# Optimization experiments

Hardware: AMD Instinct MI355X
Metric: run time of the kernel (lower is better)

Reference implementation:

```python
import jax, jax.numpy as jnp
from jax import lax
import numpy as np

T, B, IN, H = 192, 16, 256, 256


def setup_inputs() -> dict:
    key = jax.random.key(0)
    ks = jax.random.split(key, 8)
    s = 0.05  # small init scale to keep gates well-conditioned
    return {
        "x": jax.random.normal(ks[0], (T, B, IN), dtype=jnp.float32),
        # shared LSTM (PyTorch gate order i,f,g,o)
        "W_ih": jax.random.normal(ks[1], (4 * H, IN), dtype=jnp.float32) * s,
        "W_hh": jax.random.normal(ks[2], (4 * H, H), dtype=jnp.float32) * s,
        "b_lstm": jnp.zeros((4 * H,), dtype=jnp.float32),
        # additive attention: Ws: (IN+2H)->H, Us: H->1
        "Ws_w": jax.random.normal(ks[3], (H, IN + 2 * H), dtype=jnp.float32) * s,
        "Ws_b": jnp.zeros((H,), dtype=jnp.float32),
        "Us_w": jax.random.normal(ks[4], (1, H), dtype=jnp.float32) * s,
        "Us_b": jnp.zeros((1,), dtype=jnp.float32),
        # task-specific message LSTM cell: gates from concat(x_t, Rt, h_prev)
        "Wc": jax.random.normal(ks[5], (4 * H, IN + 2 * H), dtype=jnp.float32) * s,
        "bc": jnp.zeros((4 * H,), dtype=jnp.float32),
        "TASK": 0,
    }


def _lstm_gates(pre, c):
    i, f, g, o = jnp.split(pre, 4, axis=-1)
    i = jax.nn.sigmoid(i)
    f = jax.nn.sigmoid(f)
    g = jnp.tanh(g)
    o = jax.nn.sigmoid(o)
    c_new = f * c + i * g
    h_new = o * jnp.tanh(c_new)
    return h_new, c_new


def reference(x, W_ih, W_hh, b_lstm, Ws_w, Ws_b, Us_w, Us_b, Wc, bc, TASK):
    t_len, b, _ = x.shape
    h = W_hh.shape[1]

    h0 = jnp.zeros((b, h), x.dtype)

    # ---- shared LSTM over time ----
    def shared_step(carry, xt):
        hh, cc = carry
        pre = xt @ W_ih.T + hh @ W_hh.T + b_lstm
        hh, cc = _lstm_gates(pre, cc)
        return (hh, cc), hh

    (_, _), hs = lax.scan(shared_step, (h0, h0), x)  # hs: [T,B,H]

    # ---- per-timestep additive attention + message LSTM cell ----
    def task_step(carry, xt):
        hh, cc = carry
        h_task = jnp.broadcast_to(hh[None], (t_len, b, h))
        cat = jnp.concatenate([hs, h_task, x], axis=-1)          # [T,B,IN+2H]
        score = jnp.tanh(cat @ Ws_w.T + Ws_b) @ Us_w.T + Us_b    # [T,B,1]
        att = jax.nn.softmax(score, axis=0)                       # over time
        Rt = jnp.sum(att * hs, axis=0)                            # [B,H]
        pre = jnp.concatenate([xt, Rt, hh], axis=-1) @ Wc.T + bc
        hh, cc = _lstm_gates(pre, cc)
        return (hh, cc), hh

    (_, _), outs = lax.scan(task_step, (h0, h0), x)  # [T,B,H]
    return jnp.transpose(outs, (1, 0, 2))  # [B,T,H] (torch.stack axis=1)
```

## Files before the change

kernel.cpp:

```cpp
#include <hip/hip_runtime.h>
#include <hip/hip_fp16.h>

#define T_LEN 192

typedef unsigned long long u64;
typedef _Float16 f16x8 __attribute__((ext_vector_type(8)));
typedef float f32x4 __attribute__((ext_vector_type(4)));

#define OFF_X1F   0
#define OFF_XPRE  3145728
#define OFF_XB3   6291456
#define OFF_HSB   7077888
#define OFF_P     7864320
#define OFF_H     7921664
#define OFF_HX    7929856
#define OFF_HP    7946240
#define EXCH_WORDS 147456

#define SMEM_TASK 148736

__device__ __forceinline__ unsigned packh2(float a, float b){
  union { __half2 h; unsigned u; } v;
  v.h = __halves2half2(__float2half(a), __float2half(b));
  return v.u;
}
__device__ __forceinline__ float2 unp2(unsigned u){
  union { unsigned u32; __half2 h; } v; v.u32 = u;
  return __half22float2(v.h);
}
__device__ __forceinline__ float fdot2(unsigned a, unsigned b, float c){
#if __has_builtin(__builtin_amdgcn_fdot2)
  typedef _Float16 h2t __attribute__((ext_vector_type(2)));
  union { unsigned u; h2t h; } ua, ub;
  ua.u = a; ub.u = b;
  return __builtin_amdgcn_fdot2(ua.h, ub.h, c, false);
#else
  float2 x = unp2(a), y = unp2(b);
  return c + x.x*y.x + x.y*y.y;
#endif
}
__device__ __forceinline__ float tanh_f(float x){
  float cx = fminf(fmaxf(x, -15.f), 15.f);
  float e = __expf(2.f * cx);
  return (e - 1.f) / (e + 1.f);
}
__device__ __forceinline__ float sigm(float x){
  float cx = fminf(fmaxf(x, -30.f), 30.f);
  return 1.f / (1.f + __expf(-cx));
}

__device__ __forceinline__ u64 gld64(const u64* p){
  return __hip_atomic_load(p, __ATOMIC_RELAXED, __HIP_MEMORY_SCOPE_AGENT);
}
__device__ __forceinline__ void gst64(u64* p, u64 v){
  __hip_atomic_store(p, v, __ATOMIC_RELAXED, __HIP_MEMORY_SCOPE_AGENT);
}

__global__ __launch_bounds__(256) void initk(float* p, int n){
  int i = blockIdx.x * blockDim.x + threadIdx.x;
  int stride = gridDim.x * blockDim.x;
  for (; i < n; i += stride) p[i] = 0.f;
}

__global__ __launch_bounds__(256) void proj3m(const float* __restrict__ x,
                                              const float* __restrict__ W_ih,
                                              const float* __restrict__ b_l,
                                              const float* __restrict__ Wc,
                                              const float* __restrict__ bc,
                                              const float* __restrict__ Ws_w,
                                              const float* __restrict__ Ws_b,
                                              float* __restrict__ ws){
  __shared__ unsigned xhi[2][16 * 136];
  __shared__ unsigned xlo[2][16 * 136];
  const int bx = blockIdx.x, t0 = blockIdx.y * 2, tid = threadIdx.x;

  #pragma unroll
  for (int tt = 0; tt < 2; ++tt) {
    int row = tid >> 4, c0 = (tid & 15) * 16;
    const float* xp = &x[((t0 + tt) * 16 + row) * 256 + c0];
    #pragma unroll
    for (int i = 0; i < 8; ++i) {
      float2 v = *(const float2*)&xp[2 * i];
      _Float16 h0 = (_Float16)v.x, h1 = (_Float16)v.y;
      float l0 = v.x - (float)h0, l1 = v.y - (float)h1;
      union { _Float16 h[2]; unsigned u; } ph, pl;
      ph.h[0] = h0; ph.h[1] = h1;
      pl.h[0] = (_Float16)l0; pl.h[1] = (_Float16)l1;
      xhi[tt][row * 136 + c0 / 2 + i] = ph.u;
      xlo[tt][row * 136 + c0 / 2 + i] = pl.u;
    }
  }

  const int wave = tid >> 6, lane = tid & 63;
  const int b16 = lane & 15, quad = lane >> 4;
  const int n0 = bx * 64 + wave * 16;
  const float* wrow; const float* bias; int nb, mode;
  if (bx < 16)      { nb = n0;        wrow = &W_ih[(nb + b16) * 256];       bias = b_l;  mode = 0; }
  else if (bx < 32) { nb = n0 - 1024; wrow = &Wc[(nb + b16) * 768];         bias = bc;   mode = 1; }
  else              { nb = n0 - 2048; wrow = &Ws_w[(nb + b16) * 768 + 512]; bias = Ws_b; mode = 2; }

  f16x8 whi[8], wlo[8];
  #pragma unroll
  for (int kk = 0; kk < 8; ++kk) {
    const float* wp = wrow + kk * 32 + quad * 8;
    f16x8 h, l;
    #pragma unroll
    for (int j = 0; j < 8; ++j) {
      float v = wp[j];
      _Float16 hh = (_Float16)v;
      h[j] = hh; l[j] = (_Float16)(v - (float)hh);
    }
    whi[kk] = h; wlo[kk] = l;
  }
  f32x4 acc[2];
  #pragma unroll
  for (int tt = 0; tt < 2; ++tt)
    #pragma unroll
    for (int r = 0; r < 4; ++r) acc[tt][r] = bias[nb + quad * 4 + r];
  __syncthreads();

  #pragma unroll
  for (int kk = 0; kk < 8; ++kk) {
    #pragma unroll
    for (int tt = 0; tt < 2; ++tt) {
      union { uint4 u; f16x8 h; } bh, bl;
      bh.u = *(const uint4*)&xhi[tt][b16 * 136 + kk * 16 + quad * 4];
      bl.u = *(const uint4*)&xlo[tt][b16 * 136 + kk * 16 + quad * 4];
      acc[tt] = __builtin_amdgcn_mfma_f32_16x16x32_f16(whi[kk], bh.h, acc[tt], 0, 0, 0);
      acc[tt] = __builtin_amdgcn_mfma_f32_16x16x32_f16(wlo[kk], bh.h, acc[tt], 0, 0, 0);
      acc[tt] = __builtin_amdgcn_mfma_f32_16x16x32_f16(whi[kk], bl.h, acc[tt], 0, 0, 0);
    }
  }

  #pragma unroll
  for (int tt = 0; tt < 2; ++tt) {
    int t = t0 + tt;
    float4 res; res.x = acc[tt][0]; res.y = acc[tt][1]; res.z = acc[tt][2]; res.w = acc[tt][3];
    if (mode == 0) {
      *(float4*)&ws[OFF_X1F + (((u64)t * 64 + (n0 >> 4)) * 16 + b16) * 16 + quad * 4] = res;
    } else if (mode == 1) {
      *(float4*)&ws[OFF_XPRE + ((u64)t * 16 + b16) * 1024 + nb + quad * 4] = res;
    } else {
      *(float4*)&ws[OFF_XB3 + ((u64)t * 16 + b16) * 256 + nb + quad * 4] = res;
    }
  }
}

__global__ __launch_bounds__(512) void lstm_kernel(const float* __restrict__ X1F,
                                                   const float* __restrict__ W_hh,
                                                   float* __restrict__ hsB,
                                                   u64* __restrict__ hx){
  __shared__ unsigned hT[16 * 136];
  const int tid = threadIdx.x;
  const int wg = blockIdx.x;
  const int wave = tid >> 6, lane = tid & 63;
  const int b16 = lane & 15, quad = lane >> 4;
  const int jb = wg * 8 + wave;
  const int peerbase = (1 - wg) * 64;

  f16x8 wf[4][8];
  #pragma unroll
  for (int g = 0; g < 4; ++g) {
    #pragma unroll
    for (int kk = 0; kk < 8; ++kk) {
      int row = g * 256 + jb * 16 + b16;
      const float* wp = &W_hh[row * 256 + kk * 32 + quad * 8];
      f16x8 v;
      #pragma unroll
      for (int j = 0; j < 8; ++j) v[j] = (_Float16)wp[j];
      wf[g][kk] = v;
    }
  }
  for (int i = tid; i < 16 * 136; i += 512) hT[i] = 0u;
  float cst[4] = {0.f, 0.f, 0.f, 0.f};
  __syncthreads();

  for (int t = 0; t < T_LEN; ++t) {
    float4 xi[4];
    #pragma unroll
    for (int g = 0; g < 4; ++g)
      xi[g] = *(const float4*)&X1F[((t * 64 + g * 16 + jb) * 16 + b16) * 16 + quad * 4];

    if (t > 0) {
      const u64* src = &hx[((u64)((t - 1) & 1)) * 2048];
      int bbq = tid >> 5, k2 = tid & 31;
      int jp0 = peerbase + 2 * k2;
      u64 v0 = gld64(&src[bbq * 128 + jp0]);
      u64 v1 = gld64(&src[bbq * 128 + jp0 + 1]);
      while ((unsigned)v0 != (unsigned)t || (unsigned)v1 != (unsigned)t) {
        __builtin_amdgcn_s_sleep(1);
        v0 = gld64(&src[bbq * 128 + jp0]);
        v1 = gld64(&src[bbq * 128 + jp0 + 1]);
      }
      hT[bbq * 136 + jp0]     = (unsigned)(v0 >> 32);
      hT[bbq * 136 + jp0 + 1] = (unsigned)(v1 >> 32);
    }
    __syncthreads();

    f32x4 acc[4];
    #pragma unroll
    for (int g = 0; g < 4; ++g) {
      f32x4 a; a[0]=xi[g].x; a[1]=xi[g].y; a[2]=xi[g].z; a[3]=xi[g].w;
      acc[g] = a;
    }
    #pragma unroll
    for (int kk = 0; kk < 8; ++kk) {
      union { uint4 u; f16x8 h; } bv;
      bv.u = *(const uint4*)&hT[b16 * 136 + kk * 16 + quad * 4];
      #pragma unroll
      for (int g = 0; g < 4; ++g)
        acc[g] = __builtin_amdgcn_mfma_f32_16x16x32_f16(wf[g][kk], bv.h, acc[g], 0, 0, 0);
    }
    __syncthreads();

    float hv[4];
    #pragma unroll
    for (int r = 0; r < 4; ++r) {
      float pi = acc[0][r], pf = acc[1][r], pg = acc[2][r], po = acc[3][r];
      float cn = fmaf(sigm(pf), cst[r], sigm(pi) * tanh_f(pg));
      hv[r] = sigm(po) * tanh_f(cn);
      cst[r] = cn;
    }
    int j0 = jb * 16 + quad * 4;
    int jp = j0 >> 1;
    unsigned p01 = packh2(hv[0], hv[1]);
    unsigned p23 = packh2(hv[2], hv[3]);
    u64* dst = &hx[((u64)(t & 1)) * 2048];
    gst64(&dst[b16 * 128 + jp],     ((u64)p01 << 32) | (unsigned)(t + 1));
    gst64(&dst[b16 * 128 + jp + 1], ((u64)p23 << 32) | (unsigned)(t + 1));
    *(float4*)&hsB[(b16 * 192 + t) * 256 + j0] = make_float4(hv[0], hv[1], hv[2], hv[3]);
    hT[b16 * 136 + jp]     = p01;
    hT[b16 * 136 + jp + 1] = p23;
  }
}

__global__ __launch_bounds__(1024) void task_kernel(
    const float* __restrict__ xb3, const float* __restrict__ xpre,
    const float* __restrict__ hsB, const float* __restrict__ Us_w,
    const float* __restrict__ Us_b, const float* __restrict__ Wc,
    const float* __restrict__ Ws_w,
    u64* __restrict__ Pbuf, u64* __restrict__ Hbuf, u64* __restrict__ HPbuf,
    float* __restrict__ out){
  extern __shared__ char smem[];
  unsigned* hsL  = (unsigned*)smem;
  unsigned* Ws1L = (unsigned*)(smem + 99072);
  float*    baseS= (float*)(smem + 115584);
  unsigned* WcH  = (unsigned*)smem;
  unsigned* Ws2P = (unsigned*)(smem + 65536);
  float* prel    = (float*)(smem + 82944);
  float* eel     = (float*)(smem + 89600);
  unsigned* h2l  = (unsigned*)(smem + 90368);
  unsigned* h2own= (unsigned*)(smem + 90880);
  float* hterml  = (float*)(smem + 90944);
  float* usl     = (float*)(smem + 91072);
  float* msc     = (float*)(smem + 91200);
  unsigned* G2   = (unsigned*)(smem + 99072);

  const int tid = threadIdx.x;
  const int bb = blockIdx.x & 15;
  const int s  = blockIdx.x >> 4;

  for (int idx = tid; idx < 24576; idx += 1024) {
    int tp = idx >> 7, k2 = idx & 127;
    const float* hp = &hsB[(bb * 192 + tp) * 256 + 2 * k2];
    hsL[tp * 129 + k2] = packh2(hp[0], hp[1]);
  }
  for (int idx = tid; idx < 4096; idx += 1024) {
    int c = idx >> 7, k2 = idx & 127;
    const float* wp = &Ws_w[(32 * s + c) * 768 + 2 * k2];
    Ws1L[c * 129 + k2] = packh2(wp[0], wp[1]);
  }
  __syncthreads();
  {
    int c = tid & 31, g = tid >> 5;
    float a6[6];
    #pragma unroll
    for (int j = 0; j < 6; ++j)
      a6[j] = xb3[((g * 6 + j) * 16 + bb) * 256 + 32 * s + c];
    for (int k2 = 0; k2 < 128; ++k2) {
      unsigned wv = Ws1L[c * 129 + k2];
      #pragma unroll
      for (int j = 0; j < 6; ++j)
        a6[j] = fdot2(wv, hsL[(g * 6 + j) * 129 + k2], a6[j]);
    }
    #pragma unroll
    for (int j = 0; j < 6; ++j)
      baseS[(g * 6 + j) * 33 + c] = a6[j];
  }
  __syncthreads();
  unsigned bs4[4] = {0u, 0u, 0u, 0u};
  if (tid < 768) {
    int tp = tid >> 2, q = tid & 3;
    #pragma unroll
    for (int j2 = 0; j2 < 4; ++j2)
      bs4[j2] = packh2(baseS[tp * 33 + q * 8 + 2 * j2],
                       baseS[tp * 33 + q * 8 + 2 * j2 + 1]);
  }
  __syncthreads();
  {
    int l = tid & 127, tg = tid >> 7;
    int row = (l >> 5) * 256 + 32 * s + (l & 31);
    const float* wr = &Wc[row * 768 + 256];
    float acc[24];
    #pragma unroll
    for (int i = 0; i < 24; ++i) acc[i] = 0.f;
    for (int kc = 0; kc < 128; kc += 16) {
      unsigned wv[16];
      #pragma unroll
      for (int i = 0; i < 16; ++i) {
        float2 wp2 = *(const float2*)&wr[2 * (kc + i)];
        wv[i] = packh2(wp2.x, wp2.y);
      }
      #pragma unroll
      for (int tt = 0; tt < 24; ++tt) {
        const unsigned* hp = &hsL[(tg * 24 + tt) * 129 + kc];
        float a = acc[tt];
        #pragma unroll
        for (int i = 0; i < 16; ++i) a = fdot2(wv[i], hp[i], a);
        acc[tt] = a;
      }
    }
    #pragma unroll
    for (int i = 0; i < 12; ++i)
      G2[l * 97 + tg * 12 + i] = packh2(acc[2 * i], acc[2 * i + 1]);
  }
  __syncthreads();
  for (int idx = tid; idx < 16384; idx += 1024) {
    int j = idx & 3, l = (idx >> 2) & 127, k2q = idx >> 9;
    int k2 = k2q * 4 + j;
    int row = (l >> 5) * 256 + 32 * s + (l & 31);
    const float* wp = &Wc[row * 768 + 512 + 2 * k2];
    WcH[idx] = packh2(wp[0], wp[1]);
  }
  for (int idx = tid; idx < 4096; idx += 1024) {
    int c = idx >> 4, j = idx & 15;
    const float* wp = &Ws_w[c * 768 + 256 + 2 * (16 * s + j)];
    Ws2P[c * 17 + j] = packh2(wp[0], wp[1]);
  }
  if (tid < 32) usl[tid] = Us_w[32 * s + tid];
  const float usb = Us_b[0];
  __syncthreads();

  u64* Pb  = Pbuf + (bb * 8) * 192;
  u64* Hb  = Hbuf + bb * 256;
  u64* HPb = HPbuf + (bb * 8) * 256;
  const uint4* wp4 = (const uint4*)WcH;
  const uint4* av4 = (const uint4*)h2l;
  float creg = 0.f;

  for (int t = 0; t < T_LEN; ++t) {
    const unsigned seq = (unsigned)(t + 1);
    float xp0 = 0.f, xp1 = 0.f, xp2 = 0.f, xp3 = 0.f;
    if (tid < 32) {
      const float* xq = &xpre[(t * 16 + bb) * 1024 + 32 * s + tid];
      xp0 = xq[0]; xp1 = xq[256]; xp2 = xq[512]; xp3 = xq[768];
    }
    if (t > 0) {
      if (tid < 256) {
        int c = tid >> 3, sp = tid & 7;
        u64 v = gld64(&HPb[sp * 256 + 32 * s + c]);
        while ((unsigned)v != (unsigned)t) {
          __builtin_amdgcn_s_sleep(1);
          v = gld64(&HPb[sp * 256 + 32 * s + c]);
        }
        float a = __uint_as_float((unsigned)(v >> 32));
        a += __shfl_xor(a, 1); a += __shfl_xor(a, 2); a += __shfl_xor(a, 4);
        if (sp == 0) hterml[c] = a;
      } else if (tid < 512) {
        int col = tid - 256;
        u64 v = gld64(&Hb[col]);
        while ((unsigned)v != (unsigned)t) {
          __builtin_amdgcn_s_sleep(1);
          v = gld64(&Hb[col]);
        }
        float hvv = __uint_as_float((unsigned)(v >> 32));
        float hp_ = __shfl_xor(hvv, 1);
        if ((col & 1) == 0) h2l[col >> 1] = packh2(hvv, hp_);
      }
    } else {
      if (tid < 32) hterml[tid] = 0.f;
      if (tid < 128) h2l[tid] = 0u;
    }
    __syncthreads();
    if (tid < 768) {
      int tp = tid >> 2, q = tid & 3;
      float p = 0.f;
      #pragma unroll
      for (int m = 0; m < 4; ++m) {
        float2 bv = unp2(bs4[m]);
        int c0 = q * 8 + 2 * m;
        p += usl[c0]     * tanh_f(bv.x + hterml[c0]);
        p += usl[c0 + 1] * tanh_f(bv.y + hterml[c0 + 1]);
      }
      p += __shfl_xor(p, 1);
      p += __shfl_xor(p, 2);
      if ((tid & 3) == 0)
        gst64(&Pb[s * 192 + tp], ((u64)__float_as_uint(p) << 32) | seq);
    }
    {
      int l = tid & 127, kq = tid >> 7;
      float a = 0.f;
      #pragma unroll
      for (int i = 0; i < 4; ++i) {
        uint4 w4 = wp4[(kq * 4 + i) * 128 + l];
        uint4 a4 = av4[kq * 4 + i];
        a = fdot2(w4.x, a4.x, a); a = fdot2(w4.y, a4.y, a);
        a = fdot2(w4.z, a4.z, a); a = fdot2(w4.w, a4.w, a);
      }
      prel[l * 13 + kq] = a;
    }
    if (tid < 192) {
      u64 v[8];
      for (;;) {
        bool ok = true;
        #pragma unroll
        for (int sp = 0; sp < 8; ++sp) {
          v[sp] = gld64(&Pb[sp * 192 + tid]);
          ok &= ((unsigned)v[sp] == seq);
        }
        if (ok) break;
        __builtin_amdgcn_s_sleep(1);
      }
      float sum = 0.f;
      #pragma unroll
      for (int sp = 0; sp < 8; ++sp) sum += __uint_as_float((unsigned)(v[sp] >> 32));
      eel[tid] = __expf(sum + usb);
    }
    __syncthreads();
    if (tid < 64) {
      float aa = eel[tid] + eel[tid + 64] + eel[tid + 128];
      #pragma unroll
      for (int off = 32; off >= 1; off >>= 1) aa += __shfl_xor(aa, off);
      if (tid == 0) msc[0] = 1.f / aa;
    }
    if (tid >= 512) {
      int l = (tid - 512) & 127, tq = (tid - 512) >> 7;
      const unsigned* gp = &G2[l * 97 + tq * 24];
      const float2* ep = (const float2*)&eel[tq * 48];
      float a = 0.f;
      #pragma unroll
      for (int i = 0; i < 24; ++i) {
        float2 g = unp2(gp[i]);
        float2 e = ep[i];
        a = fmaf(g.x, e.x, a); a = fmaf(g.y, e.y, a);
      }
      prel[l * 13 + 8 + tq] = a;
    }
    __syncthreads();
    if (tid < 32) {
      float m = msc[0];
      float pr[4];
      #pragma unroll
      for (int g = 0; g < 4; ++g) {
        const float* pp = &prel[(g * 32 + tid) * 13];
        float hsum = pp[0] + pp[1] + pp[2] + pp[3] + pp[4] + pp[5] + pp[6] + pp[7];
        float gsum = pp[8] + pp[9] + pp[10] + pp[11];
        pr[g] = hsum + m * gsum;
      }
      pr[0] += xp0; pr[1] += xp1; pr[2] += xp2; pr[3] += xp3;
      float cn = fmaf(sigm(pr[1]), creg, sigm(pr[0]) * tanh_f(pr[2]));
      float hh = sigm(pr[3]) * tanh_f(cn);
      creg = cn;
      gst64(&Hb[32 * s + tid], ((u64)__float_as_uint(hh) << 32) | seq);
      out[(bb * 192 + t) * 256 + 32 * s + tid] = hh;
      float hp_ = __shfl_xor(hh, 1);
      if ((tid & 1) == 0) h2own[tid >> 1] = packh2(hh, hp_);
    }
    __syncthreads();
    if (tid < 256) {
      float a = 0.f;
      const unsigned* wp = &Ws2P[tid * 17];
      #pragma unroll
      for (int j = 0; j < 16; ++j) a = fdot2(wp[j], h2own[j], a);
      gst64(&HPb[s * 256 + tid], ((u64)__float_as_uint(a) << 32) | seq);
    }
  }
}

extern "C" void kernel_launch(void* const* d_in, const int* in_sizes, int n_in,
                              void* d_out, int out_size, void* d_ws, size_t ws_size,
                              hipStream_t stream) {
  (void)in_sizes; (void)n_in; (void)out_size; (void)ws_size;
  const float* x    = (const float*)d_in[0];
  const float* W_ih = (const float*)d_in[1];
  const float* W_hh = (const float*)d_in[2];
  const float* b_l  = (const float*)d_in[3];
  const float* Ws_w = (const float*)d_in[4];
  const float* Ws_b = (const float*)d_in[5];
  const float* Us_w = (const float*)d_in[6];
  const float* Us_b = (const float*)d_in[7];
  const float* Wc   = (const float*)d_in[8];
  const float* bc   = (const float*)d_in[9];
  float* out = (float*)d_out;
  float* ws = (float*)d_ws;

  hipFuncSetAttribute((const void*)task_kernel,
                      hipFuncAttributeMaxDynamicSharedMemorySize, 160 * 1024);

  initk<<<64, 256, 0, stream>>>(ws + OFF_P, EXCH_WORDS);

  proj3m<<<dim3(36, 96), 256, 0, stream>>>(x, W_ih, b_l, Wc, bc, Ws_w, Ws_b, ws);

  lstm_kernel<<<2, 512, 0, stream>>>(ws + OFF_X1F, W_hh, ws + OFF_HSB,
                                     (u64*)(ws + OFF_HX));

  task_kernel<<<128, 1024, SMEM_TASK, stream>>>(
      ws + OFF_XB3, ws + OFF_XPRE, ws + OFF_HSB, Us_w, Us_b, Wc, Ws_w,
      (u64*)(ws + OFF_P), (u64*)(ws + OFF_H), (u64*)(ws + OFF_HP), out);
}
```

Before: 1.630 ms.

## Co-locate LSTM workgroups on one XCD and poll flags with sc0 loads

```diff
diff --git a/kernel.cpp b/kernel.cpp
--- a/kernel.cpp
+++ b/kernel.cpp
@@ -14,6 +14,7 @@
 #define OFF_P     7864320
 #define OFF_H     7921664
 #define OFF_HX    7929856
+#define OFF_TICKET 7938048
 #define OFF_HP    7946240
 #define EXCH_WORDS 147456
 
@@ -54,6 +55,30 @@
 }
 __device__ __forceinline__ void gst64(u64* p, u64 v){
   __hip_atomic_store(p, v, __ATOMIC_RELAXED, __HIP_MEMORY_SCOPE_AGENT);
+}
+__device__ __forceinline__ u64 ld64_sc0(const u64* p){
+  u64 v;
+  asm volatile("global_load_dwordx2 %0, %1, off sc0\n\ts_waitcnt vmcnt(0)"
+               : "=v"(v) : "v"(p) : "memory");
+  return v;
+}
+__device__ __forceinline__ void st64_sc0(u64* p, u64 v){
+  asm volatile("global_store_dwordx2 %0, %1, off sc0" :: "v"(p), "v"(v) : "memory");
+}
+__device__ __forceinline__ void pub64(u64* p, u64 v){
+  gst64(p, v);
+  st64_sc0(p, v);
+}
+__device__ __forceinline__ u64 poll_tag(const u64* p, unsigned want){
+  for (int k = 1; ; ++k) {
+    u64 v = ld64_sc0(p);
+    if ((unsigned)v == want) return v;
+    if ((k & 7) == 0) {
+      v = gld64(p);
+      if ((unsigned)v == want) return v;
+      __builtin_amdgcn_s_sleep(1);
+    }
+  }
 }
 
 __global__ __launch_bounds__(256) void initk(float* p, int n){
@@ -149,10 +174,35 @@
 __global__ __launch_bounds__(512) void lstm_kernel(const float* __restrict__ X1F,
                                                    const float* __restrict__ W_hh,
                                                    float* __restrict__ hsB,
-                                                   u64* __restrict__ hx){
+                                                   u64* __restrict__ hx,
+                                                   unsigned* __restrict__ ticket){
   __shared__ unsigned hT[16 * 136];
+  __shared__ int role_s;
   const int tid = threadIdx.x;
-  const int wg = blockIdx.x;
+
+  if (tid == 0) {
+    int xcc = (int)__builtin_amdgcn_s_getreg(20 | (31 << 11)) & 7;
+    unsigned slot = __hip_atomic_fetch_add(&ticket[xcc], 1u,
+                        __ATOMIC_RELAXED, __HIP_MEMORY_SCOPE_AGENT);
+    int role = -1;
+    if (slot < 2u) {
+      if (slot == 1u) {
+        unsigned expv = 0u;
+        __hip_atomic_compare_exchange_strong(&ticket[8], &expv, (unsigned)(xcc + 1),
+            __ATOMIC_RELAXED, __ATOMIC_RELAXED, __HIP_MEMORY_SCOPE_AGENT);
+      }
+      unsigned ch;
+      do {
+        ch = __hip_atomic_load(&ticket[8], __ATOMIC_RELAXED, __HIP_MEMORY_SCOPE_AGENT);
+      } while (ch == 0u);
+      if (ch == (unsigned)(xcc + 1)) role = (int)slot;
+    }
+    role_s = role;
+  }
+  __syncthreads();
+  const int wg = role_s;
+  if (wg < 0) return;
+
   const int wave = tid >> 6, lane = tid & 63;
   const int b16 = lane & 15, quad = lane >> 4;
   const int jb = wg * 8 + wave;
@@ -185,12 +235,17 @@
       const u64* src = &hx[((u64)((t - 1) & 1)) * 2048];
       int bbq = tid >> 5, k2 = tid & 31;
       int jp0 = peerbase + 2 * k2;
-      u64 v0 = gld64(&src[bbq * 128 + jp0]);
-      u64 v1 = gld64(&src[bbq * 128 + jp0 + 1]);
-      while ((unsigned)v0 != (unsigned)t || (unsigned)v1 != (unsigned)t) {
-        __builtin_amdgcn_s_sleep(1);
-        v0 = gld64(&src[bbq * 128 + jp0]);
-        v1 = gld64(&src[bbq * 128 + jp0 + 1]);
+      const u64* ap = &src[bbq * 128 + jp0];
+      u64 v0, v1;
+      for (int k = 1; ; ++k) {
+        v0 = ld64_sc0(ap);
+        v1 = ld64_sc0(ap + 1);
+        if ((unsigned)v0 == (unsigned)t && (unsigned)v1 == (unsigned)t) break;
+        if ((k & 7) == 0) {
+          v0 = gld64(ap); v1 = gld64(ap + 1);
+          if ((unsigned)v0 == (unsigned)t && (unsigned)v1 == (unsigned)t) break;
+          __builtin_amdgcn_s_sleep(1);
+        }
       }
       hT[bbq * 136 + jp0]     = (unsigned)(v0 >> 32);
       hT[bbq * 136 + jp0 + 1] = (unsigned)(v1 >> 32);
@@ -226,8 +281,13 @@
     unsigned p01 = packh2(hv[0], hv[1]);
     unsigned p23 = packh2(hv[2], hv[3]);
     u64* dst = &hx[((u64)(t & 1)) * 2048];
-    gst64(&dst[b16 * 128 + jp],     ((u64)p01 << 32) | (unsigned)(t + 1));
-    gst64(&dst[b16 * 128 + jp + 1], ((u64)p23 << 32) | (unsigned)(t + 1));
+    u64* ap = &dst[b16 * 128 + jp];
+    u64 r0 = ((u64)p01 << 32) | (unsigned)(t + 1);
+    u64 r1 = ((u64)p23 << 32) | (unsigned)(t + 1);
+    gst64(ap, r0);
+    gst64(ap + 1, r1);
+    st64_sc0(ap, r0);
+    st64_sc0(ap + 1, r1);
     *(float4*)&hsB[(b16 * 192 + t) * 256 + j0] = make_float4(hv[0], hv[1], hv[2], hv[3]);
     hT[b16 * 136 + jp]     = p01;
     hT[b16 * 136 + jp + 1] = p23;
@@ -358,21 +418,13 @@
     if (t > 0) {
       if (tid < 256) {
         int c = tid >> 3, sp = tid & 7;
-        u64 v = gld64(&HPb[sp * 256 + 32 * s + c]);
-        while ((unsigned)v != (unsigned)t) {
-          __builtin_amdgcn_s_sleep(1);
-          v = gld64(&HPb[sp * 256 + 32 * s + c]);
-        }
+        u64 v = poll_tag(&HPb[sp * 256 + 32 * s + c], (unsigned)t);
         float a = __uint_as_float((unsigned)(v >> 32));
         a += __shfl_xor(a, 1); a += __shfl_xor(a, 2); a += __shfl_xor(a, 4);
         if (sp == 0) hterml[c] = a;
       } else if (tid < 512) {
         int col = tid - 256;
-        u64 v = gld64(&Hb[col]);
-        while ((unsigned)v != (unsigned)t) {
-          __builtin_amdgcn_s_sleep(1);
-          v = gld64(&Hb[col]);
-        }
+        u64 v = poll_tag(&Hb[col], (unsigned)t);
         float hvv = __uint_as_float((unsigned)(v >> 32));
         float hp_ = __shfl_xor(hvv, 1);
         if ((col & 1) == 0) h2l[col >> 1] = packh2(hvv, hp_);
@@ -395,7 +447,7 @@
       p += __shfl_xor(p, 1);
       p += __shfl_xor(p, 2);
       if ((tid & 3) == 0)
-        gst64(&Pb[s * 192 + tp], ((u64)__float_as_uint(p) << 32) | seq);
+        pub64(&Pb[s * 192 + tp], ((u64)__float_as_uint(p) << 32) | seq);
     }
     {
       int l = tid & 127, kq = tid >> 7;
@@ -410,20 +462,51 @@
       prel[l * 13 + kq] = a;
     }
     if (tid < 192) {
-      u64 v[8];
-      for (;;) {
-        bool ok = true;
-        #pragma unroll
-        for (int sp = 0; sp < 8; ++sp) {
-          v[sp] = gld64(&Pb[sp * 192 + tid]);
-          ok &= ((unsigned)v[sp] == seq);
+      const u64 *q0 = &Pb[0 * 192 + tid], *q1 = &Pb[1 * 192 + tid];
+      const u64 *q2 = &Pb[2 * 192 + tid], *q3 = &Pb[3 * 192 + tid];
+      const u64 *q4 = &Pb[4 * 192 + tid], *q5 = &Pb[5 * 192 + tid];
+      const u64 *q6 = &Pb[6 * 192 + tid], *q7 = &Pb[7 * 192 + tid];
+      u64 v0, v1, v2, v3, v4, v5, v6, v7;
+      for (int k = 1; ; ++k) {
+        asm volatile(
+          "global_load_dwordx2 %0, %8, off sc0\n\t"
+          "global_load_dwordx2 %1, %9, off sc0\n\t"
+          "global_load_dwordx2 %2, %10, off sc0\n\t"
+          "global_load_dwordx2 %3, %11, off sc0\n\t"
+          "global_load_dwordx2 %4, %12, off sc0\n\t"
+          "global_load_dwordx2 %5, %13, off sc0\n\t"
+          "global_load_dwordx2 %6, %14, off sc0\n\t"
+          "global_load_dwordx2 %7, %15, off sc0\n\t"
+          "s_waitcnt vmcnt(0)"
+          : "=&v"(v0), "=&v"(v1), "=&v"(v2), "=&v"(v3),
+            "=&v"(v4), "=&v"(v5), "=&v"(v6), "=&v"(v7)
+          : "v"(q0), "v"(q1), "v"(q2), "v"(q3),
+            "v"(q4), "v"(q5), "v"(q6), "v"(q7)
+          : "memory");
+        bool ok = (unsigned)v0 == seq && (unsigned)v1 == seq &&
+                  (unsigned)v2 == seq && (unsigned)v3 == seq &&
+                  (unsigned)v4 == seq && (unsigned)v5 == seq &&
+                  (unsigned)v6 == seq && (unsigned)v7 == seq;
+        if (ok) break;
+        if ((k & 7) == 0) {
+          v0 = gld64(q0); v1 = gld64(q1); v2 = gld64(q2); v3 = gld64(q3);
+          v4 = gld64(q4); v5 = gld64(q5); v6 = gld64(q6); v7 = gld64(q7);
+          ok = (unsigned)v0 == seq && (unsigned)v1 == seq &&
+               (unsigned)v2 == seq && (unsigned)v3 == seq &&
+               (unsigned)v4 == seq && (unsigned)v5 == seq &&
+               (unsigned)v6 == seq && (unsigned)v7 == seq;
+          if (ok) break;
+          __builtin_amdgcn_s_sleep(1);
         }
-        if (ok) break;
-        __builtin_amdgcn_s_sleep(1);
-      }
-      float sum = 0.f;
-      #pragma unroll
-      for (int sp = 0; sp < 8; ++sp) sum += __uint_as_float((unsigned)(v[sp] >> 32));
+      }
+      float sum = __uint_as_float((unsigned)(v0 >> 32)) +
+                  __uint_as_float((unsigned)(v1 >> 32)) +
+                  __uint_as_float((unsigned)(v2 >> 32)) +
+                  __uint_as_float((unsigned)(v3 >> 32)) +
+                  __uint_as_float((unsigned)(v4 >> 32)) +
+                  __uint_as_float((unsigned)(v5 >> 32)) +
+                  __uint_as_float((unsigned)(v6 >> 32)) +
+                  __uint_as_float((unsigned)(v7 >> 32));
       eel[tid] = __expf(sum + usb);
     }
     __syncthreads();
@@ -461,7 +544,7 @@
       float cn = fmaf(sigm(pr[1]), creg, sigm(pr[0]) * tanh_f(pr[2]));
       float hh = sigm(pr[3]) * tanh_f(cn);
       creg = cn;
-      gst64(&Hb[32 * s + tid], ((u64)__float_as_uint(hh) << 32) | seq);
+      pub64(&Hb[32 * s + tid], ((u64)__float_as_uint(hh) << 32) | seq);
       out[(bb * 192 + t) * 256 + 32 * s + tid] = hh;
       float hp_ = __shfl_xor(hh, 1);
       if ((tid & 1) == 0) h2own[tid >> 1] = packh2(hh, hp_);
@@ -472,7 +555,7 @@
       const unsigned* wp = &Ws2P[tid * 17];
       #pragma unroll
       for (int j = 0; j < 16; ++j) a = fdot2(wp[j], h2own[j], a);
-      gst64(&HPb[s * 256 + tid], ((u64)__float_as_uint(a) << 32) | seq);
+      pub64(&HPb[s * 256 + tid], ((u64)__float_as_uint(a) << 32) | seq);
     }
   }
 }
@@ -494,15 +577,16 @@
   float* out = (float*)d_out;
   float* ws = (float*)d_ws;
 
-  hipFuncSetAttribute((const void*)task_kernel,
-                      hipFuncAttributeMaxDynamicSharedMemorySize, 160 * 1024);
+  (void)hipFuncSetAttribute((const void*)task_kernel,
+                            hipFuncAttributeMaxDynamicSharedMemorySize, 160 * 1024);
 
   initk<<<64, 256, 0, stream>>>(ws + OFF_P, EXCH_WORDS);
 
   proj3m<<<dim3(36, 96), 256, 0, stream>>>(x, W_ih, b_l, Wc, bc, Ws_w, Ws_b, ws);
 
-  lstm_kernel<<<2, 512, 0, stream>>>(ws + OFF_X1F, W_hh, ws + OFF_HSB,
-                                     (u64*)(ws + OFF_HX));
+  lstm_kernel<<<16, 512, 0, stream>>>(ws + OFF_X1F, W_hh, ws + OFF_HSB,
+                                      (u64*)(ws + OFF_HX),
+                                      (unsigned*)(ws + OFF_TICKET));
 
   task_kernel<<<128, 1024, SMEM_TASK, stream>>>(
       ws + OFF_XB3, ws + OFF_XPRE, ws + OFF_HSB, Us_w, Us_b, Wc, Ws_w,
```

Measured after the change: 2.363 ms. 1.45x slower.
